# Optimization experiments

Measured on AMD Instinct MI355X. Metric: run time of the kernel, lower is better.

## Reference

```python
import jax, jax.numpy as jnp
import numpy as np

SP = 4          # split_size
HEADS = 8       # num_heads
SHIFTS = (0, 2) # shift_sizes


def _to_windows(t, nh, hs, nw, ws, heads):
    # 'b (c head) (nh hs) (nw ws) -> (b nh nw) head (hs ws) c'
    B, C, H, W = t.shape
    hd = C // heads
    t = t.reshape(B, hd, heads, nh, hs, nw, ws)
    t = t.transpose(0, 3, 5, 2, 4, 6, 1)  # B, nh, nw, heads, hs, ws, hd
    return t.reshape(B * nh * nw, heads, hs * ws, hd)


def _from_windows(t, B, nh, hs, nw, ws, heads):
    # '(b nh nw) head (hs ws) c -> b (c head) (nh hs) (nw ws)'
    hd = t.shape[-1]
    t = t.reshape(B, nh, nw, heads, hs, ws, hd)
    t = t.transpose(0, 6, 3, 1, 4, 2, 5)  # B, hd, heads, nh, hs, nw, ws
    return t.reshape(B, hd * heads, nh * hs, nw * ws)


def _dwconv3(v, w, b):
    # depthwise 3x3, padding 1 (groups = channels)
    out = jax.lax.conv_general_dilated(
        v, w, window_strides=(1, 1), padding=((1, 1), (1, 1)),
        dimension_numbers=('NCHW', 'OIHW', 'NCHW'),
        feature_group_count=v.shape[1])
    return out + b[None, :, None, None]


def setup_inputs() -> dict:
    key = jax.random.key(0)
    k1, k2, k3, k4 = jax.random.split(key, 4)
    B, C, H, W = 8, 256, 64, 64
    sd = C // 2
    x = jax.random.normal(k1, (B, C, H, W), dtype=jnp.float32)
    w_qkv = jax.random.normal(k2, (3 * sd, sd, 1, 1), dtype=jnp.float32) * 0.05
    w_lepe = jax.random.normal(k3, (sd, 1, 3, 3), dtype=jnp.float32) * 0.1
    b_lepe = jax.random.normal(k4, (sd,), dtype=jnp.float32) * 0.01
    return {"x": x, "w_qkv": w_qkv, "w_lepe": w_lepe, "b_lepe": b_lepe}


def reference(x, w_qkv, w_lepe, b_lepe):
    B, C, H, W = x.shape
    sd = C // 2
    scale = (sd // HEADS) ** -0.5
    wq = w_qkv[:, :, 0, 0]  # [3*sd, sd]
    outs = []
    for s in SHIFTS:
        # NOTE: original rolls dims (1,2) = (channels, height)
        xs = jnp.roll(x, (-s, -s), axis=(1, 2)) if s > 0 else x
        parts = []
        # vertical strips (full-H, width SP), horizontal strips (height SP, full-W)
        strip_params = [(1, H, W // SP, SP), (H // SP, SP, 1, W)]
        for idx, (nh, hs, nw, ws) in enumerate(strip_params):
            xsp = xs[:, idx * sd:(idx + 1) * sd]  # channel half
            qkv = jnp.einsum('bchw,oc->bohw', xsp, wq)
            q, k, v = qkv[:, :sd], qkv[:, sd:2 * sd], qkv[:, 2 * sd:]
            lepe = _dwconv3(v, w_lepe, b_lepe)
            qw = _to_windows(q, nh, hs, nw, ws, HEADS) * scale
            kw = _to_windows(k, nh, hs, nw, ws, HEADS)
            vw = _to_windows(v, nh, hs, nw, ws, HEADS)
            lw = _to_windows(lepe, nh, hs, nw, ws, HEADS)
            attn = jax.nn.softmax(jnp.einsum('whqc,whkc->whqk', qw, kw), axis=-1)
            ow = jnp.einsum('whqk,whkc->whqc', attn, vw) + lw
            o = _from_windows(ow, B, nh, hs, nw, ws, HEADS)
            if s > 0:
                o = jnp.roll(o, (s, s), axis=(1, 2))
            parts.append(o)
        outs.append(jnp.concatenate(parts, axis=1))
    return outs[0] + outs[1]
```

## Files before the change

kernel.cpp:

```cpp
#include <hip/hip_runtime.h>
#include <hip/hip_bf16.h>

typedef _Float16 f16;
typedef _Float16 half4 __attribute__((ext_vector_type(4)));
typedef float floatx4 __attribute__((ext_vector_type(4)));

#define WIN 4194304
#define SSTR 41943040

__global__ void k_prep(const float* __restrict__ wq, f16* __restrict__ wqB) {
    int D = blockIdx.x * 256 + threadIdx.x;
    if (D >= 49152) return;
    int kj = D & 3, lane = (D >> 2) & 63, nt = (D >> 8) & 7;
    int kt = (D >> 11) & 7, part = D >> 14;
    int g = lane >> 4, ln = lane & 15;
    int o = part * 128 + nt * 16 + ln;
    int k = kt * 16 + g * 4 + kj;
    wqB[D] = (f16)wq[o * 128 + k];
}

__global__ __launch_bounds__(256, 2) void k_proj(
    const float* __restrict__ x, const f16* __restrict__ wqB,
    f16* __restrict__ qw, f16* __restrict__ kw, f16* __restrict__ vw)
{
    const int rt = blockIdx.x, b = blockIdx.y;
    const int idx = blockIdx.z & 1, si = blockIdx.z >> 1;
    const int s = si * 2;
    const size_t so = (size_t)si * SSTR;
    const int h0 = rt * 2;
    const int tid = threadIdx.x;
    const int wave = tid >> 6, lane = tid & 63, g = lane >> 4, ln = lane & 15;

    union __align__(16) SM {
        f16 xa[32 * 128 * 4];
        f16 pt[128 * 136];
    };
    __shared__ SM sm;

    {
        const int wg = tid & 31;
        const int row = wg >> 4, w4 = (wg & 15) << 2;
        const int gh = (h0 + row + s) & 63;
        const int m0 = row * 64 + w4;
        const unsigned fb = (((unsigned)m0 >> 4) & 7u) << 4;
        const float* xp = x + (((size_t)b * 256) << 12) + (gh << 6) + w4;
        char* lbase = (char*)sm.xa;
        #pragma unroll
        for (int it = 0; it < 4; ++it) {
            int cg = (tid >> 5) + it * 8;
            float4 v4[4];
            #pragma unroll
            for (int cc = 0; cc < 4; ++cc) {
                int gc = (idx * 128 + cg * 4 + cc + s) & 255;
                v4[cc] = *(const float4*)(xp + ((size_t)gc << 12));
            }
            union { half4 h[4]; float4 q[2]; } t;
            #pragma unroll
            for (int jj = 0; jj < 4; ++jj)
                t.h[jj] = (half4){
                    (f16)(((const float*)&v4[0])[jj]),
                    (f16)(((const float*)&v4[1])[jj]),
                    (f16)(((const float*)&v4[2])[jj]),
                    (f16)(((const float*)&v4[3])[jj])};
            char* p = lbase + cg * 1024;
            *(float4*)(p + (((unsigned)(m0 * 8)) ^ fb)) = t.q[0];
            *(float4*)(p + (((unsigned)(m0 * 8 + 16)) ^ fb)) = t.q[1];
        }
    }
    __syncthreads();

    half4 af[2][8];
    #pragma unroll
    for (int mt = 0; mt < 2; ++mt) {
        int m = wave * 32 + mt * 16 + ln;
        unsigned fb = (((unsigned)m >> 4) & 7u) << 4;
        #pragma unroll
        for (int kt = 0; kt < 8; ++kt) {
            int kc = kt * 4 + g;
            af[mt][kt] = *(const half4*)((char*)sm.xa + kc * 1024 +
                                         (((unsigned)(m * 8)) ^ fb));
        }
    }

    for (int part = 0; part < 3; ++part) {
        floatx4 C[8][2];
        #pragma unroll
        for (int nt = 0; nt < 8; ++nt)
            #pragma unroll
            for (int mt = 0; mt < 2; ++mt) C[nt][mt] = (floatx4){0.f, 0.f, 0.f, 0.f};

        for (int kt = 0; kt < 8; ++kt) {
            half4 bf[8];
            #pragma unroll
            for (int nt = 0; nt < 8; ++nt)
                bf[nt] = *(const half4*)&wqB[((((part * 8 + kt) * 8 + nt) * 64) + lane) * 4];
            #pragma unroll
            for (int nt = 0; nt < 8; ++nt)
                #pragma unroll
                for (int mt = 0; mt < 2; ++mt)
                    C[nt][mt] = __builtin_amdgcn_mfma_f32_16x16x16f16(
                        af[mt][kt], bf[nt], C[nt][mt], 0, 0, 0);
        }

        const float qsc = (part == 0) ? 0.25f * 1.4426950408889634f : 1.0f;

        __syncthreads();
        #pragma unroll
        for (int nt = 0; nt < 8; ++nt)
            #pragma unroll
            for (int mt = 0; mt < 2; ++mt)
                #pragma unroll
                for (int r = 0; r < 4; ++r) {
                    int m = wave * 32 + mt * 16 + g * 4 + r;
                    int c = nt * 16 + ln;
                    int hc = ((c & 7) << 4) + (c >> 3);
                    f16 hv = (f16)(C[nt][mt][r] * qsc);
                    if (part == 2) sm.pt[hc * 136 + m] = hv;
                    else           sm.pt[m * 136 + hc] = hv;
                }
        __syncthreads();

        if (part < 2) {
            f16* dst = (part == 0 ? qw : kw) + so + (size_t)idx * WIN;
            int tq = tid >> 4, hcg = tid & 15;
            #pragma unroll
            for (int it = 0; it < 8; ++it) {
                int m = it * 16 + tq;
                int h = h0 + (m >> 6), w = m & 63;
                int winG, t;
                if (idx == 0) { winG = b * 16 + (w >> 2); t = (h << 2) | (w & 3); }
                else          { winG = b * 16 + (h >> 2); t = ((h & 3) << 6) | w; }
                *(float4*)(dst + (((size_t)winG * 256 + t) << 7) + hcg * 8) =
                    *(const float4*)&sm.pt[m * 136 + hcg * 8];
            }
        } else {
            f16* dst = vw + so + (size_t)idx * WIN;
            int mg = tid & 15, hcq = tid >> 4;
            int row = mg >> 3, h = h0 + row;
            #pragma unroll
            for (int it = 0; it < 8; ++it) {
                int hc = it * 16 + hcq;
                if (idx == 1) {
                    int w = (mg & 7) * 8;
                    int winG = b * 16 + (h >> 2);
                    int t = ((h & 3) << 6) | w;
                    *(float4*)(dst + (((size_t)winG * 128 + hc) << 8) + t) =
                        *(const float4*)&sm.pt[hc * 136 + mg * 8];
                } else {
                    #pragma unroll
                    for (int q2 = 0; q2 < 2; ++q2) {
                        int w0 = (mg & 7) * 8 + q2 * 4;
                        int winG = b * 16 + (w0 >> 2);
                        int t = h << 2;
                        *(half4*)(dst + (((size_t)winG * 128 + hc) << 8) + t) =
                            *(const half4*)&sm.pt[hc * 136 + mg * 8 + q2 * 4];
                    }
                }
            }
        }
    }
}

__global__ __launch_bounds__(256) void k_lepe(
    const f16* __restrict__ vw, const float* __restrict__ wle,
    const float* __restrict__ ble, f16* __restrict__ lepe)
{
    const int winG = blockIdx.x, hg = blockIdx.z;
    const int idx = blockIdx.y & 1, si = blockIdx.y >> 1;
    const size_t so = (size_t)si * SSTR;
    const int wi = winG & 15;
    const int tid = threadIdx.x;
    const int hc0 = hg * 8;
    const f16* vb = vw + so + (size_t)idx * WIN;
    f16* lb = lepe + so + (size_t)idx * WIN;

    __shared__ f16 sp[4096];

    if (idx == 0) {
        for (int ii = tid; ii < 8 * 256; ii += 256) {
            int hcl = ii >> 8, t = ii & 255;
            f16 v = vb[(((size_t)winG * 128 + hc0 + hcl) << 8) + t];
            sp[(hcl << 9) + ((t >> 2) << 3) + 1 + (t & 3)] = v;
        }
        for (int ii = tid; ii < 8 * 128; ii += 256) {
            int hcl = ii >> 7, j = ii & 127;
            int side = j >> 6, h = j & 63;
            f16 v = (f16)0.f;
            if (side == 0) { if (wi > 0)
                v = vb[(((size_t)(winG - 1) * 128 + hc0 + hcl) << 8) + h * 4 + 3]; }
            else           { if (wi < 15)
                v = vb[(((size_t)(winG + 1) * 128 + hc0 + hcl) << 8) + h * 4]; }
            sp[(hcl << 9) + (h << 3) + (side ? 5 : 0)] = v;
        }
        __syncthreads();
        int h = tid >> 2, wp = 1 + (tid & 3);
        for (int hcl = 0; hcl < 8; ++hcl) {
            int hc = hc0 + hcl, d = hc & 15, head = hc >> 4;
            int c = d * 8 + head;
            float acc = ble[c];
            #pragma unroll
            for (int ky = 0; ky < 3; ++ky) {
                int hh = h + ky - 1;
                if (hh < 0 || hh > 63) continue;
                #pragma unroll
                for (int kx = 0; kx < 3; ++kx)
                    acc = fmaf(wle[c * 9 + ky * 3 + kx],
                               (float)sp[(hcl << 9) + (hh << 3) + wp + kx - 1], acc);
            }
            lb[(((size_t)winG * 128 + hc) << 8) + tid] = (f16)acc;
        }
    } else {
        const int ROW = 68;
        for (int ii = tid; ii < 8 * 256; ii += 256) {
            int hcl = ii >> 8, t = ii & 255;
            f16 v = vb[(((size_t)winG * 128 + hc0 + hcl) << 8) + t];
            sp[hcl * 6 * ROW + (1 + (t >> 6)) * ROW + 1 + (t & 63)] = v;
        }
        for (int ii = tid; ii < 8 * 128; ii += 256) {
            int hcl = ii >> 7, j = ii & 127;
            int side = j >> 6, w = j & 63;
            f16 v = (f16)0.f;
            if (side == 0) { if (wi > 0)
                v = vb[(((size_t)(winG - 1) * 128 + hc0 + hcl) << 8) + 192 + w]; }
            else           { if (wi < 15)
                v = vb[(((size_t)(winG + 1) * 128 + hc0 + hcl) << 8) + w]; }
            sp[hcl * 6 * ROW + (side ? 5 : 0) * ROW + 1 + w] = v;
        }
        for (int ii = tid; ii < 8 * 6 * 2; ii += 256) {
            int hcl = ii / 12, rr = (ii % 12) >> 1, e = ii & 1;
            sp[hcl * 6 * ROW + rr * ROW + (e ? 65 : 0)] = (f16)0.f;
        }
        __syncthreads();
        int hloc = tid >> 6, w = tid & 63;
        for (int hcl = 0; hcl < 8; ++hcl) {
            int hc = hc0 + hcl, d = hc & 15, head = hc >> 4;
            int c = d * 8 + head;
            float acc = ble[c];
            #pragma unroll
            for (int ky = 0; ky < 3; ++ky)
                #pragma unroll
                for (int kx = 0; kx < 3; ++kx)
                    acc = fmaf(wle[c * 9 + ky * 3 + kx],
                               (float)sp[hcl * 6 * ROW + (hloc + ky) * ROW + w + kx],
                               acc);
            lb[(((size_t)winG * 128 + hc) << 8) + tid] = (f16)acc;
        }
    }
}

__global__ __launch_bounds__(256) void k_attn(
    const f16* __restrict__ qw, const f16* __restrict__ kw,
    const f16* __restrict__ vw, const f16* __restrict__ lep,
    f16* __restrict__ ow)
{
    const int tid = threadIdx.x;
    const int lane = tid & 63, wave = tid >> 6;
    const int g = lane >> 4, ln = lane & 15;
    const int head = blockIdx.x & 7, idx = (blockIdx.x >> 3) & 1;
    const int winG = (blockIdx.x >> 4) & 127;
    const int si = blockIdx.x >> 11;
    const size_t so = (size_t)si * SSTR;

    __shared__ f16 kl[4096];
    __shared__ f16 vl[4096];

    const size_t cb = ((size_t)(winG * 8 + head)) << 4;
    const f16* qb = qw + so + (size_t)idx * WIN + ((size_t)winG << 15) + head * 16;
    const f16* kb = kw + so + (size_t)idx * WIN + ((size_t)winG << 15) + head * 16;
    const f16* vb = vw + so + (size_t)idx * WIN;
    const f16* lb = lep + so + (size_t)idx * WIN;
    f16* ob = ow + so + (size_t)idx * WIN;

    {
        int t = tid;
        const f16* src = kb + ((size_t)t << 7);
        float4 a = *(const float4*)src;
        float4 b2 = *(const float4*)(src + 8);
        const f16* ap = (const f16*)&a;
        const f16* bp = (const f16*)&b2;
        int kt = t >> 4, l2 = t & 15;
        *(half4*)&kl[(kt * 64 + 0 * 16 + l2) * 4] = *(const half4*)(ap);
        *(half4*)&kl[(kt * 64 + 1 * 16 + l2) * 4] = *(const half4*)(ap + 4);
        *(half4*)&kl[(kt * 64 + 2 * 16 + l2) * 4] = *(const half4*)(bp);
        *(half4*)&kl[(kt * 64 + 3 * 16 + l2) * 4] = *(const half4*)(bp + 4);
    }
    {
        const f16* src = vb + (cb << 8);
        #pragma unroll
        for (int r2 = 0; r2 < 2; ++r2) {
            int e = r2 * 256 + tid;
            float4 a = *(const float4*)(src + e * 8);
            const f16* ap = (const f16*)&a;
            int d = e >> 5;
            int t0 = (e & 31) * 8;
            int kt0 = t0 >> 4, g0 = (t0 >> 2) & 3;
            *(half4*)&vl[(kt0 * 64 + g0 * 16 + d) * 4] = *(const half4*)ap;
            int t1 = t0 + 4;
            int kt1 = t1 >> 4, g1 = (t1 >> 2) & 3;
            *(half4*)&vl[(kt1 * 64 + g1 * 16 + d) * 4] = *(const half4*)(ap + 4);
        }
    }

    half4 qf[4];
    #pragma unroll
    for (int qt = 0; qt < 4; ++qt) {
        int t = wave * 64 + qt * 16 + ln;
        qf[qt] = *(const half4*)(qb + ((size_t)t << 7) + g * 4);
    }

    __syncthreads();

    floatx4 o[4]; float lsum[4];
    #pragma unroll
    for (int qt = 0; qt < 4; ++qt) { o[qt] = (floatx4){0.f,0.f,0.f,0.f}; lsum[qt] = 0.f; }

    for (int kt = 0; kt < 16; ++kt) {
        half4 kf = *(const half4*)&kl[(kt * 64 + lane) * 4];
        half4 vf = *(const half4*)&vl[(kt * 64 + lane) * 4];
        #pragma unroll
        for (int qt = 0; qt < 4; ++qt) {
            floatx4 sc = __builtin_amdgcn_mfma_f32_16x16x16f16(
                kf, qf[qt], (floatx4){0.f,0.f,0.f,0.f}, 0, 0, 0);
            float p0 = __builtin_amdgcn_exp2f(sc[0]);
            float p1 = __builtin_amdgcn_exp2f(sc[1]);
            float p2 = __builtin_amdgcn_exp2f(sc[2]);
            float p3 = __builtin_amdgcn_exp2f(sc[3]);
            lsum[qt] += (p0 + p1) + (p2 + p3);
            half4 pf = {(f16)p0, (f16)p1, (f16)p2, (f16)p3};
            o[qt] = __builtin_amdgcn_mfma_f32_16x16x16f16(vf, pf, o[qt], 0, 0, 0);
        }
    }

    #pragma unroll
    for (int qt = 0; qt < 4; ++qt) {
        float l = lsum[qt];
        l += __shfl_xor(l, 16);
        l += __shfl_xor(l, 32);
        float inv = 1.f / l;
        int t = wave * 64 + qt * 16 + ln;
        #pragma unroll
        for (int r = 0; r < 4; ++r) {
            int d = g * 4 + r;
            float val = fmaf(o[qt][r], inv, (float)lb[((cb + d) << 8) + t]);
            ob[((cb + d) << 8) + t] = (f16)val;
        }
    }
}

__global__ __launch_bounds__(256) void k_final(
    const f16* __restrict__ ow0, const f16* __restrict__ ow2,
    float* __restrict__ out)
{
    __shared__ f16 sp[2][16][68];
    const int tid = threadIdx.x;
    const int e0 = blockIdx.x << 10;
    const int oc = (e0 >> 12) & 255, bb = e0 >> 20, oh0 = (e0 >> 6) & 63;
    const int idx = oc >> 7;

    if (idx == 0) {
        #pragma unroll
        for (int si = 0; si < 2; ++si) {
            const f16* p = si ? ow2 : ow0;
            int s = si * 2;
            int cl = ((oc & 127) - s) & 127;
            int head = cl & 7, d = cl >> 3;
            #pragma unroll
            for (int it = 0; it < 4; ++it) {
                int v = it * 256 + tid;
                int k = v >> 6, j = v & 63;
                int t = (((oh0 + (j >> 2) - s) & 63) << 2) | (j & 3);
                int wg = bb * 16 + k;
                sp[si][k][j] =
                    p[(((size_t)(wg * 8 + head) * 16 + d) << 8) + t];
            }
        }
        __syncthreads();
        #pragma unroll
        for (int it = 0; it < 4; ++it) {
            int e = e0 + it * 256 + tid;
            int w = e & 63, oh = (e >> 6) & 63;
            int j = ((oh - oh0) << 2) | (w & 3);
            float acc = (float)sp[0][w >> 2][j] + (float)sp[1][w >> 2][j];
            out[e] = acc;
        }
    } else {
        #pragma unroll
        for (int it = 0; it < 4; ++it) {
            int e = e0 + it * 256 + tid;
            int w = e & 63, oh = (e >> 6) & 63;
            float acc = 0.f;
            #pragma unroll
            for (int si = 0; si < 2; ++si) {
                int s = si * 2;
                const f16* p = si ? ow2 : ow0;
                int cl = ((oc & 127) - s) & 127;
                int h = (oh - s) & 63;
                int head = cl & 7, d = cl >> 3;
                int wg = bb * 16 + (h >> 2);
                int t = ((h & 3) << 6) | w;
                acc += (float)p[(size_t)WIN
                                + (((size_t)(wg * 8 + head) * 16 + d) << 8) + t];
            }
            out[e] = acc;
        }
    }
}

extern "C" void kernel_launch(void* const* d_in, const int* in_sizes, int n_in,
                              void* d_out, int out_size, void* d_ws, size_t ws_size,
                              hipStream_t stream) {
    const float* x      = (const float*)d_in[0];
    const float* w_qkv  = (const float*)d_in[1];
    const float* w_lepe = (const float*)d_in[2];
    const float* b_lepe = (const float*)d_in[3];
    float* out = (float*)d_out;

    f16* wsf = (f16*)d_ws;
    f16* wqB  = wsf;
    f16* base = wsf + 65536;
    f16* qw   = base;
    f16* kw   = base + 2 * (size_t)WIN;
    f16* vw   = base + 4 * (size_t)WIN;
    f16* lep  = base + 6 * (size_t)WIN;
    f16* ow   = base + 8 * (size_t)WIN;

    k_prep<<<192, 256, 0, stream>>>(w_qkv, wqB);

    k_proj<<<dim3(32, 8, 4), 256, 0, stream>>>(x, wqB, qw, kw, vw);
    k_lepe<<<dim3(128, 4, 16), 256, 0, stream>>>(vw, w_lepe, b_lepe, lep);
    k_attn<<<4096, 256, 0, stream>>>(qw, kw, vw, lep, ow);

    k_final<<<8192, 256, 0, stream>>>(ow, ow + (size_t)SSTR, out);
}
```

Before: 230.5 us.

## Fuse depthwise LePE convolution into attention kernel, drop separate lepe pass

Removes the standalone k_lepe kernel and computes the 3x3 depthwise convolution inside k_attn. Each attention block stages its head's 16 V channels plus halo into shared memory, convolves them after the attention loop, and adds the result from LDS in the epilogue. This avoids writing and re-reading the lepe buffer in global memory and saves one launch. In exchange shared memory grows to 32KB per block, which may reduce occupancy, and two extra barriers plus the conv arithmetic now sit inside the attention kernel.

```diff
diff --git a/kernel.cpp b/kernel.cpp
--- a/kernel.cpp
+++ b/kernel.cpp
@@ -161,97 +161,10 @@
     }
 }
 
-__global__ __launch_bounds__(256) void k_lepe(
-    const f16* __restrict__ vw, const float* __restrict__ wle,
-    const float* __restrict__ ble, f16* __restrict__ lepe)
-{
-    const int winG = blockIdx.x, hg = blockIdx.z;
-    const int idx = blockIdx.y & 1, si = blockIdx.y >> 1;
-    const size_t so = (size_t)si * SSTR;
-    const int wi = winG & 15;
-    const int tid = threadIdx.x;
-    const int hc0 = hg * 8;
-    const f16* vb = vw + so + (size_t)idx * WIN;
-    f16* lb = lepe + so + (size_t)idx * WIN;
-
-    __shared__ f16 sp[4096];
-
-    if (idx == 0) {
-        for (int ii = tid; ii < 8 * 256; ii += 256) {
-            int hcl = ii >> 8, t = ii & 255;
-            f16 v = vb[(((size_t)winG * 128 + hc0 + hcl) << 8) + t];
-            sp[(hcl << 9) + ((t >> 2) << 3) + 1 + (t & 3)] = v;
-        }
-        for (int ii = tid; ii < 8 * 128; ii += 256) {
-            int hcl = ii >> 7, j = ii & 127;
-            int side = j >> 6, h = j & 63;
-            f16 v = (f16)0.f;
-            if (side == 0) { if (wi > 0)
-                v = vb[(((size_t)(winG - 1) * 128 + hc0 + hcl) << 8) + h * 4 + 3]; }
-            else           { if (wi < 15)
-                v = vb[(((size_t)(winG + 1) * 128 + hc0 + hcl) << 8) + h * 4]; }
-            sp[(hcl << 9) + (h << 3) + (side ? 5 : 0)] = v;
-        }
-        __syncthreads();
-        int h = tid >> 2, wp = 1 + (tid & 3);
-        for (int hcl = 0; hcl < 8; ++hcl) {
-            int hc = hc0 + hcl, d = hc & 15, head = hc >> 4;
-            int c = d * 8 + head;
-            float acc = ble[c];
-            #pragma unroll
-            for (int ky = 0; ky < 3; ++ky) {
-                int hh = h + ky - 1;
-                if (hh < 0 || hh > 63) continue;
-                #pragma unroll
-                for (int kx = 0; kx < 3; ++kx)
-                    acc = fmaf(wle[c * 9 + ky * 3 + kx],
-                               (float)sp[(hcl << 9) + (hh << 3) + wp + kx - 1], acc);
-            }
-            lb[(((size_t)winG * 128 + hc) << 8) + tid] = (f16)acc;
-        }
-    } else {
-        const int ROW = 68;
-        for (int ii = tid; ii < 8 * 256; ii += 256) {
-            int hcl = ii >> 8, t = ii & 255;
-            f16 v = vb[(((size_t)winG * 128 + hc0 + hcl) << 8) + t];
-            sp[hcl * 6 * ROW + (1 + (t >> 6)) * ROW + 1 + (t & 63)] = v;
-        }
-        for (int ii = tid; ii < 8 * 128; ii += 256) {
-            int hcl = ii >> 7, j = ii & 127;
-            int side = j >> 6, w = j & 63;
-            f16 v = (f16)0.f;
-            if (side == 0) { if (wi > 0)
-                v = vb[(((size_t)(winG - 1) * 128 + hc0 + hcl) << 8) + 192 + w]; }
-            else           { if (wi < 15)
-                v = vb[(((size_t)(winG + 1) * 128 + hc0 + hcl) << 8) + w]; }
-            sp[hcl * 6 * ROW + (side ? 5 : 0) * ROW + 1 + w] = v;
-        }
-        for (int ii = tid; ii < 8 * 6 * 2; ii += 256) {
-            int hcl = ii / 12, rr = (ii % 12) >> 1, e = ii & 1;
-            sp[hcl * 6 * ROW + rr * ROW + (e ? 65 : 0)] = (f16)0.f;
-        }
-        __syncthreads();
-        int hloc = tid >> 6, w = tid & 63;
-        for (int hcl = 0; hcl < 8; ++hcl) {
-            int hc = hc0 + hcl, d = hc & 15, head = hc >> 4;
-            int c = d * 8 + head;
-            float acc = ble[c];
-            #pragma unroll
-            for (int ky = 0; ky < 3; ++ky)
-                #pragma unroll
-                for (int kx = 0; kx < 3; ++kx)
-                    acc = fmaf(wle[c * 9 + ky * 3 + kx],
-                               (float)sp[hcl * 6 * ROW + (hloc + ky) * ROW + w + kx],
-                               acc);
-            lb[(((size_t)winG * 128 + hc) << 8) + tid] = (f16)acc;
-        }
-    }
-}
-
 __global__ __launch_bounds__(256) void k_attn(
     const f16* __restrict__ qw, const f16* __restrict__ kw,
-    const f16* __restrict__ vw, const f16* __restrict__ lep,
-    f16* __restrict__ ow)
+    const f16* __restrict__ vw, const float* __restrict__ wle,
+    const float* __restrict__ ble, f16* __restrict__ ow)
 {
     const int tid = threadIdx.x;
     const int lane = tid & 63, wave = tid >> 6;
@@ -260,15 +173,18 @@
     const int winG = (blockIdx.x >> 4) & 127;
     const int si = blockIdx.x >> 11;
     const size_t so = (size_t)si * SSTR;
-
-    __shared__ f16 kl[4096];
-    __shared__ f16 vl[4096];
+    const int wi = winG & 15;
+
+    __shared__ f16 smem[16384];
+    f16* kl = smem;
+    f16* vl = smem + 4096;
+    f16* sp = smem + 8192;
+    f16* co = smem;
 
     const size_t cb = ((size_t)(winG * 8 + head)) << 4;
     const f16* qb = qw + so + (size_t)idx * WIN + ((size_t)winG << 15) + head * 16;
     const f16* kb = kw + so + (size_t)idx * WIN + ((size_t)winG << 15) + head * 16;
     const f16* vb = vw + so + (size_t)idx * WIN;
-    const f16* lb = lep + so + (size_t)idx * WIN;
     f16* ob = ow + so + (size_t)idx * WIN;
 
     {
@@ -300,6 +216,44 @@
             *(half4*)&vl[(kt1 * 64 + g1 * 16 + d) * 4] = *(const half4*)(ap + 4);
         }
     }
+    if (idx == 0) {
+        for (int ii = tid; ii < 16 * 256; ii += 256) {
+            int hcl = ii >> 8, t = ii & 255;
+            f16 v = vb[(cb << 8) + (hcl << 8) + t];
+            sp[(hcl << 9) + ((t >> 2) << 3) + 1 + (t & 3)] = v;
+        }
+        for (int ii = tid; ii < 16 * 128; ii += 256) {
+            int hcl = ii >> 7, j = ii & 127;
+            int side = j >> 6, h = j & 63;
+            f16 v = (f16)0.f;
+            if (side == 0) { if (wi > 0)
+                v = vb[(((size_t)(winG - 1) * 128 + head * 16 + hcl) << 8) + h * 4 + 3]; }
+            else           { if (wi < 15)
+                v = vb[(((size_t)(winG + 1) * 128 + head * 16 + hcl) << 8) + h * 4]; }
+            sp[(hcl << 9) + (h << 3) + (side ? 5 : 0)] = v;
+        }
+    } else {
+        const int ROW = 68;
+        for (int ii = tid; ii < 16 * 256; ii += 256) {
+            int hcl = ii >> 8, t = ii & 255;
+            f16 v = vb[(cb << 8) + (hcl << 8) + t];
+            sp[hcl * 6 * ROW + (1 + (t >> 6)) * ROW + 1 + (t & 63)] = v;
+        }
+        for (int ii = tid; ii < 16 * 128; ii += 256) {
+            int hcl = ii >> 7, j = ii & 127;
+            int side = j >> 6, w = j & 63;
+            f16 v = (f16)0.f;
+            if (side == 0) { if (wi > 0)
+                v = vb[(((size_t)(winG - 1) * 128 + head * 16 + hcl) << 8) + 192 + w]; }
+            else           { if (wi < 15)
+                v = vb[(((size_t)(winG + 1) * 128 + head * 16 + hcl) << 8) + w]; }
+            sp[hcl * 6 * ROW + (side ? 5 : 0) * ROW + 1 + w] = v;
+        }
+        for (int ii = tid; ii < 16 * 6 * 2; ii += 256) {
+            int hcl = ii / 12, rr = (ii % 12) >> 1, e = ii & 1;
+            sp[hcl * 6 * ROW + rr * ROW + (e ? 65 : 0)] = (f16)0.f;
+        }
+    }
 
     half4 qf[4];
     #pragma unroll
@@ -331,6 +285,42 @@
         }
     }
 
+    __syncthreads();
+
+    if (idx == 0) {
+        int h = tid >> 2, wp = 1 + (tid & 3);
+        for (int hcl = 0; hcl < 16; ++hcl) {
+            int c = hcl * 8 + head;
+            float acc = ble[c];
+            #pragma unroll
+            for (int ky = 0; ky < 3; ++ky) {
+                int hh = h + ky - 1;
+                if (hh < 0 || hh > 63) continue;
+                #pragma unroll
+                for (int kx = 0; kx < 3; ++kx)
+                    acc = fmaf(wle[c * 9 + ky * 3 + kx],
+                               (float)sp[(hcl << 9) + (hh << 3) + wp + kx - 1], acc);
+            }
+            co[hcl * 260 + tid] = (f16)acc;
+        }
+    } else {
+        const int ROW = 68;
+        int hloc = tid >> 6, w = tid & 63;
+        for (int hcl = 0; hcl < 16; ++hcl) {
+            int c = hcl * 8 + head;
+            float acc = ble[c];
+            #pragma unroll
+            for (int ky = 0; ky < 3; ++ky)
+                #pragma unroll
+                for (int kx = 0; kx < 3; ++kx)
+                    acc = fmaf(wle[c * 9 + ky * 3 + kx],
+                               (float)sp[hcl * 6 * ROW + (hloc + ky) * ROW + w + kx],
+                               acc);
+            co[hcl * 260 + tid] = (f16)acc;
+        }
+    }
+    __syncthreads();
+
     #pragma unroll
     for (int qt = 0; qt < 4; ++qt) {
         float l = lsum[qt];
@@ -341,7 +331,7 @@
         #pragma unroll
         for (int r = 0; r < 4; ++r) {
             int d = g * 4 + r;
-            float val = fmaf(o[qt][r], inv, (float)lb[((cb + d) << 8) + t]);
+            float val = fmaf(o[qt][r], inv, (float)co[d * 260 + t]);
             ob[((cb + d) << 8) + t] = (f16)val;
         }
     }
@@ -421,14 +411,12 @@
     f16* qw   = base;
     f16* kw   = base + 2 * (size_t)WIN;
     f16* vw   = base + 4 * (size_t)WIN;
-    f16* lep  = base + 6 * (size_t)WIN;
     f16* ow   = base + 8 * (size_t)WIN;
 
     k_prep<<<192, 256, 0, stream>>>(w_qkv, wqB);
 
     k_proj<<<dim3(32, 8, 4), 256, 0, stream>>>(x, wqB, qw, kw, vw);
-    k_lepe<<<dim3(128, 4, 16), 256, 0, stream>>>(vw, w_lepe, b_lepe, lep);
-    k_attn<<<4096, 256, 0, stream>>>(qw, kw, vw, lep, ow);
+    k_attn<<<4096, 256, 0, stream>>>(qw, kw, vw, w_lepe, b_lepe, ow);
 
     k_final<<<8192, 256, 0, stream>>>(ow, ow + (size_t)SSTR, out);
 }
```

Measured after the change: 219.7 us. -4.7%, faster.
